# Kernel tuning notes

Hardware: AMD Instinct MI355X
Metric: run time of the kernel (lower is better)

Reference implementation:

```python
import jax, jax.numpy as jnp
import numpy as np
import math

DIM = 1536; NH = 12; HD = 128
F, H, W = 6, 30, 30
S = F * H * W
B = 1
K_LEN = 9900  # hardcoded k_lens in the source forward
EPS_NORM = 1e-6


def _rope_tables(max_len=1024, d=HD):
    # Wan rope_params: three tables of widths d-4*(d//6), 2*(d//6), 2*(d//6)
    # -> cos/sin tables of half-widths 22, 21, 21 (concat = d//2 = 64)
    def ang(dd):
        inv = 1.0 / (10000.0 ** (np.arange(0, dd, 2, dtype=np.float64) / dd))
        return np.outer(np.arange(max_len, dtype=np.float64), inv)
    a = np.concatenate([ang(d - 4 * (d // 6)), ang(2 * (d // 6)), ang(2 * (d // 6))], axis=1)
    return np.cos(a).astype(np.float32), np.sin(a).astype(np.float32)


def setup_inputs() -> dict:
    key = jax.random.key(0)
    ks = jax.random.split(key, 5)
    s = 1.0 / math.sqrt(DIM)
    cos, sin = _rope_tables()
    return {
        "x": jax.random.normal(ks[0], (B, S, DIM), jnp.float32),
        "q_w": jax.random.normal(ks[1], (DIM, DIM), jnp.float32) * s,
        "q_b": jnp.zeros((DIM,), jnp.float32),
        "k_w": jax.random.normal(ks[2], (DIM, DIM), jnp.float32) * s,
        "k_b": jnp.zeros((DIM,), jnp.float32),
        "v_w": jax.random.normal(ks[3], (DIM, DIM), jnp.float32) * s,
        "v_b": jnp.zeros((DIM,), jnp.float32),
        "o_w": jax.random.normal(ks[4], (DIM, DIM), jnp.float32) * s,
        "o_b": jnp.zeros((DIM,), jnp.float32),
        "norm_q_w": jnp.ones((DIM,), jnp.float32),
        "norm_k_w": jnp.ones((DIM,), jnp.float32),
        "freqs_cos": jnp.asarray(cos),
        "freqs_sin": jnp.asarray(sin),
        "grid_f": F, "grid_h": H, "grid_w": W,
    }


def rms_norm(x, w):
    # RMSNorm over full model dim, computed in fp32 (as in source)
    xf = x.astype(jnp.float32)
    xn = xf * jax.lax.rsqrt(jnp.mean(xf * xf, axis=-1, keepdims=True) + EPS_NORM)
    return xn.astype(x.dtype) * w


def rope_apply(x, cos, sin, f, h, w):
    # x: [B,S,N,D]; rotate consecutive pairs with 3D-factorized (f,h,w) freqs
    Bb, Ss, Nn, Dd = x.shape
    c = Dd // 2
    sp = [c - 2 * (c // 3), c // 3, c // 3]  # 22, 21, 21

    def grid(tab):
        tf = tab[:, :sp[0]]
        th = tab[:, sp[0]:sp[0] + sp[1]]
        tw = tab[:, sp[0] + sp[1]:]
        g = jnp.concatenate([
            jnp.broadcast_to(tf[:f, None, None, :], (f, h, w, sp[0])),
            jnp.broadcast_to(th[None, :h, None, :], (f, h, w, sp[1])),
            jnp.broadcast_to(tw[None, None, :w, :], (f, h, w, sp[2])),
        ], axis=-1)
        return g.reshape(f * h * w, 1, c)  # [S,1,c] (broadcast over heads)

    gc, gs = grid(cos), grid(sin)
    xp = x.astype(jnp.float32).reshape(Bb, Ss, Nn, c, 2)
    xr, xi = xp[..., 0], xp[..., 1]
    orr = xr * gc - xi * gs
    oii = xr * gs + xi * gc
    return jnp.stack([orr, oii], axis=-1).reshape(Bb, Ss, Nn, Dd).astype(x.dtype)


def attention(q, k, v, k_len):
    # full attention (window_size=(-1,-1)) with keys masked beyond k_len
    scale = 1.0 / math.sqrt(q.shape[-1])
    att = jnp.einsum('bqnd,bknd->bnqk', q, k) * scale
    valid = jnp.arange(k.shape[1]) < k_len
    att = jnp.where(valid[None, None, None, :], att, jnp.finfo(att.dtype).min)
    p = jax.nn.softmax(att, axis=-1)
    return jnp.einsum('bnqk,bknd->bqnd', p, v)


def reference(x, q_w, q_b, k_w, k_b, v_w, v_b, o_w, o_b, norm_q_w, norm_k_w, freqs_cos, freqs_sin, grid_f, grid_h, grid_w):
    Bb, Ss, _ = x.shape
    q = rms_norm(x @ q_w.T + q_b, norm_q_w).reshape(Bb, Ss, NH, HD)
    k = rms_norm(x @ k_w.T + k_b, norm_k_w).reshape(Bb, Ss, NH, HD)
    v = (x @ v_w.T + v_b).reshape(Bb, Ss, NH, HD)
    q = rope_apply(q, freqs_cos, freqs_sin, grid_f, grid_h, grid_w)
    k = rope_apply(k, freqs_cos, freqs_sin, grid_f, grid_h, grid_w)
    o = attention(q, k, v, K_LEN).reshape(Bb, Ss, NH * HD)
    return o @ o_w.T + o_b
```

## Files before the change

kernel.cpp:

```cpp
#include <hip/hip_runtime.h>

#define DIM 1536
#define NH 12
#define HD 128
#define S_LEN 5400
#define SPAD 5440
#define MPAD 5504
#define NQKV 4608
#define EPS_NORM 1e-6f

typedef __bf16 bf16_t;
typedef __bf16 bf16x8 __attribute__((ext_vector_type(8)));
typedef __bf16 bf16x4 __attribute__((ext_vector_type(4)));
typedef float  f32x4  __attribute__((ext_vector_type(4)));
typedef float  f32x16 __attribute__((ext_vector_type(16)));

#define GLOAD_LDS16(gp, lp) __builtin_amdgcn_global_load_lds( \
    (__attribute__((address_space(1))) void*)(void*)(gp),     \
    (__attribute__((address_space(3))) void*)(lp), 16, 0, 0)


__global__ __launch_bounds__(256) void cvt_x_kernel(const float* __restrict__ x,
                                                    bf16_t* __restrict__ xb) {
  size_t base = ((size_t)blockIdx.x * 256 + threadIdx.x) * 4;
  if (base >= (size_t)MPAD * DIM) return;
  size_t row = base / DIM;
  float4 v = make_float4(0.f, 0.f, 0.f, 0.f);
  if (row < S_LEN) v = *(const float4*)&x[base];
  bf16x4 o; o[0] = (__bf16)v.x; o[1] = (__bf16)v.y; o[2] = (__bf16)v.z; o[3] = (__bf16)v.w;
  *(bf16x4*)&xb[base] = o;
}

__global__ __launch_bounds__(256) void cvt_wqkv_kernel(const float* __restrict__ qw,
                                                       const float* __restrict__ kw,
                                                       const float* __restrict__ vw,
                                                       bf16_t* __restrict__ wb) {
  size_t base = ((size_t)blockIdx.x * 256 + threadIdx.x) * 4;
  if (base >= (size_t)NQKV * DIM) return;
  int row = (int)(base / DIM);
  int col = (int)(base - (size_t)row * DIM);
  const float* src; int rr = row;
  if (rr >= 3072)      { src = vw; rr -= 3072; }
  else if (rr >= 1536) { src = kw; rr -= 1536; }
  else                 { src = qw; }
  float4 v = *(const float4*)&src[(size_t)rr * DIM + col];
  bf16x4 o; o[0] = (__bf16)v.x; o[1] = (__bf16)v.y; o[2] = (__bf16)v.z; o[3] = (__bf16)v.w;
  *(bf16x4*)&wb[base] = o;
}

__global__ __launch_bounds__(256) void cvt_wo_kernel(const float* __restrict__ w,
                                                     bf16_t* __restrict__ wb) {
  size_t base = ((size_t)blockIdx.x * 256 + threadIdx.x) * 4;
  if (base >= (size_t)DIM * DIM) return;
  float4 v = *(const float4*)&w[base];
  bf16x4 o; o[0] = (__bf16)v.x; o[1] = (__bf16)v.y; o[2] = (__bf16)v.z; o[3] = (__bf16)v.w;
  *(bf16x4*)&wb[base] = o;
}


template<bool OUT_BF16>
__global__ __launch_bounds__(256) void gemm_bt_kernel(
    const bf16_t* __restrict__ A, const bf16_t* __restrict__ B, void* __restrict__ C,
    const float* __restrict__ bias0, const float* __restrict__ bias1,
    const float* __restrict__ bias2, int M, int N, int K, int Mvalid) {
  __shared__ bf16_t As[128 * 32];
  __shared__ bf16_t Bs[128 * 32];
  int tid = threadIdx.x;
  int lane = tid & 63, wave = tid >> 6, quad = lane >> 4, l16 = lane & 15;
  int m0 = blockIdx.y * 128, n0 = blockIdx.x * 128;
  int wm = (wave >> 1) * 64, wn = (wave & 1) * 64;
  const bf16_t* Ab = A + (size_t)m0 * K;
  const bf16_t* Bb = B + (size_t)n0 * K;
  f32x4 acc[4][4] = {};
  for (int kt = 0; kt < K; kt += 32) {
    __syncthreads();
#pragma unroll
    for (int i = 0; i < 2; i++) {
      int eo = (i * 256 + tid) * 8;
      int row = eo >> 5, col = eo & 31;
      GLOAD_LDS16(Ab + (size_t)row * K + kt + col, &As[eo]);
      GLOAD_LDS16(Bb + (size_t)row * K + kt + col, &Bs[eo]);
    }
    __syncthreads();
    bf16x8 af[4], bfr[4];
#pragma unroll
    for (int i = 0; i < 4; i++)
      af[i] = *(const bf16x8*)&As[(wm + i * 16 + l16) * 32 + quad * 8];
#pragma unroll
    for (int j = 0; j < 4; j++)
      bfr[j] = *(const bf16x8*)&Bs[(wn + j * 16 + l16) * 32 + quad * 8];
#pragma unroll
    for (int i = 0; i < 4; i++)
#pragma unroll
      for (int j = 0; j < 4; j++)
        acc[i][j] = __builtin_amdgcn_mfma_f32_16x16x32_bf16(af[i], bfr[j], acc[i][j], 0, 0, 0);
  }
#pragma unroll
  for (int j = 0; j < 4; j++) {
    int n = n0 + wn + j * 16 + l16;
    float bias = (n < 1536) ? bias0[n] : (n < 3072) ? bias1[n - 1536] : bias2[n - 3072];
#pragma unroll
    for (int i = 0; i < 4; i++) {
#pragma unroll
      for (int r = 0; r < 4; r++) {
        int m = m0 + wm + i * 16 + quad * 4 + r;
        float v = acc[i][j][r] + bias;
        if (OUT_BF16) {
          ((bf16_t*)C)[(size_t)m * N + n] = (__bf16)v;
        } else {
          if (m < Mvalid) ((float*)C)[(size_t)m * N + n] = v;
        }
      }
    }
  }
}


__global__ __launch_bounds__(256) void rope_qk_kernel(
    const bf16_t* __restrict__ qkv, const float* __restrict__ nqw,
    const float* __restrict__ nkw, const float* __restrict__ fcos,
    const float* __restrict__ fsin, bf16_t* __restrict__ qout,
    bf16_t* __restrict__ kout) {
  int s = blockIdx.x;
  int tid = threadIdx.x;
  bool valid = s < S_LEN;
  int f = s / 900, hh = (s / 30) % 30, ww = s % 30;
  __shared__ float red[4];
  for (int which = 0; which < 2; which++) {
    const bf16_t* src = qkv + (size_t)s * NQKV + which * DIM;
    const float* nw = which ? nkw : nqw;
    bf16_t* dst = (which ? kout : qout) + (size_t)s * DIM;
    float osc = which ? 1.0f : 0.08838834764831845f;
    float v[6]; float ss = 0.f;
#pragma unroll
    for (int i = 0; i < 6; i++) {
      v[i] = valid ? (float)src[tid * 6 + i] : 0.f;
      ss += v[i] * v[i];
    }
#pragma unroll
    for (int off = 32; off >= 1; off >>= 1) ss += __shfl_down(ss, off);
    if ((tid & 63) == 0) red[tid >> 6] = ss;
    __syncthreads();
    float tot = red[0] + red[1] + red[2] + red[3];
    float rn = rsqrtf(tot * (1.f / DIM) + EPS_NORM);
    __syncthreads();
#pragma unroll
    for (int i = 0; i < 3; i++) {
      int e0 = tid * 6 + 2 * i;
      int p = e0 >> 1;
      int cc = p & 63;
      int pos = (cc < 22) ? f : (cc < 43) ? hh : ww;
      float c = fcos[pos * 64 + cc], sn = fsin[pos * 64 + cc];
      float xr = v[2 * i] * rn * nw[e0];
      float xi = v[2 * i + 1] * rn * nw[e0 + 1];
      dst[e0]     = (__bf16)((xr * c - xi * sn) * osc);
      dst[e0 + 1] = (__bf16)((xr * sn + xi * c) * osc);
    }
  }
}


__global__ __launch_bounds__(256) void v_transpose_kernel(const bf16_t* __restrict__ qkv,
                                                          bf16_t* __restrict__ vt) {
  __shared__ bf16_t tile[64][136];
  int h = blockIdx.y, s0 = blockIdx.x * 64, tid = threadIdx.x;
#pragma unroll
  for (int it = 0; it < 4; it++) {
    int eo = (it * 256 + tid) * 8;
    int row = eo >> 7, col = eo & 127;
    int s = s0 + row;
    bf16x8 val = {};
    if (s < S_LEN) val = *(const bf16x8*)&qkv[(size_t)s * NQKV + 3072 + h * HD + col];
    *(bf16x8*)&tile[row][col] = val;
  }
  __syncthreads();
  int d = tid & 127, j0 = (tid >> 7) * 32;
  bf16x8 outv[4];
#pragma unroll
  for (int b = 0; b < 4; b++)
#pragma unroll
    for (int j = 0; j < 8; j++) outv[b][j] = tile[j0 + b * 8 + j][d];
  size_t base = ((size_t)h * HD + d) * SPAD + s0 + j0;
#pragma unroll
  for (int b = 0; b < 4; b++) *(bf16x8*)&vt[base + b * 8] = outv[b];
}


__global__ __launch_bounds__(256, 2) void flash_attn_kernel(
    const bf16_t* __restrict__ q, const bf16_t* __restrict__ k,
    const bf16_t* __restrict__ vt, bf16_t* __restrict__ o) {
  __shared__ bf16_t Ks[64 * 128];
  __shared__ bf16_t Vs[64 * 128];
  __shared__ bf16_t Pw[4][32 * 64];
  int head = blockIdx.y;
  int s0 = blockIdx.x * 128;
  int tid = threadIdx.x, w = tid >> 6, lane = tid & 63;
  int l31 = lane & 31, hh = lane >> 5;

  bf16x8 bq[8];
  {
    const bf16_t* qp = &q[(size_t)(s0 + w * 32 + l31) * DIM + head * HD + hh * 8];
#pragma unroll
    for (int kc = 0; kc < 8; kc++) bq[kc] = *(const bf16x8*)(qp + kc * 16);
  }

  float m_i = -1e30f, l_i = 0.f;
  f32x16 oacc[4] = {};

  for (int kt = 0; kt < SPAD; kt += 64) {
    __syncthreads();
#pragma unroll
    for (int it = 0; it < 4; it++) {
      int slot = it * 256 + tid;
      int row = slot >> 4, pc = slot & 15;
      int c = pc ^ (row & 15);
      GLOAD_LDS16(k + (size_t)(kt + row) * DIM + head * HD + c * 8, &Ks[slot * 8]);
    }
#pragma unroll
    for (int it = 0; it < 4; it++) {
      int slot = it * 256 + tid;
      int row = slot >> 4, pc = slot & 15;
      int cp = pc ^ (row & 15);
      int d = 2 * row + (cp >> 3);
      GLOAD_LDS16(vt + ((size_t)head * HD + d) * SPAD + kt + (cp & 7) * 8, &Vs[slot * 8]);
    }
    __syncthreads();

    f32x16 sacc[2] = {};
#pragma unroll
    for (int ns = 0; ns < 2; ns++) {
      int row = ns * 32 + l31;
#pragma unroll
      for (int kc = 0; kc < 8; kc++) {
        int pc = (kc * 2 + hh) ^ (row & 15);
        bf16x8 ak = *(const bf16x8*)&Ks[row * 128 + pc * 8];
        sacc[ns] = __builtin_amdgcn_mfma_f32_32x32x16_bf16(ak, bq[kc], sacc[ns], 0, 0, 0);
      }
    }

    if (kt + 64 > S_LEN) {
#pragma unroll
      for (int ns = 0; ns < 2; ns++)
#pragma unroll
        for (int r = 0; r < 16; r++) {
          int kvg = kt + ns * 32 + (r & 3) + 8 * (r >> 2) + 4 * hh;
          if (kvg >= S_LEN) sacc[ns][r] = -1e30f;
        }
    }

    float mx = -1e30f;
#pragma unroll
    for (int ns = 0; ns < 2; ns++)
#pragma unroll
      for (int r = 0; r < 16; r++) mx = fmaxf(mx, sacc[ns][r]);
    mx = fmaxf(mx, __shfl_xor(mx, 32));
    float mn = fmaxf(m_i, mx);
    float al = __expf(m_i - mn);
    m_i = mn;
    float rs = 0.f;
#pragma unroll
    for (int ns = 0; ns < 2; ns++)
#pragma unroll
      for (int r = 0; r < 16; r++) {
        float p = __expf(sacc[ns][r] - mn);
        rs += p;
        sacc[ns][r] = p;
      }
    rs += __shfl_xor(rs, 32);
    l_i = l_i * al + rs;
#pragma unroll
    for (int dt = 0; dt < 4; dt++)
#pragma unroll
      for (int r = 0; r < 16; r++) oacc[dt][r] *= al;

#pragma unroll
    for (int ns = 0; ns < 2; ns++)
#pragma unroll
      for (int t = 0; t < 4; t++) {
        bf16x4 pk;
#pragma unroll
        for (int r4 = 0; r4 < 4; r4++) pk[r4] = (__bf16)sacc[ns][t * 4 + r4];
        int c8 = ns * 8 + 2 * t + hh;
        int pc8 = c8 ^ (l31 & 15);
        *(bf16x4*)&Pw[w][l31 * 64 + pc8 * 4] = pk;
      }

#pragma unroll
    for (int kvc = 0; kvc < 4; kvc++) {
      int c8a = kvc * 4 + hh * 2;
      bf16x4 plo = *(const bf16x4*)&Pw[w][l31 * 64 + ((c8a) ^ (l31 & 15)) * 4];
      bf16x4 phi = *(const bf16x4*)&Pw[w][l31 * 64 + ((c8a + 1) ^ (l31 & 15)) * 4];
      bf16x8 bp;
#pragma unroll
      for (int j = 0; j < 4; j++) { bp[j] = plo[j]; bp[j + 4] = phi[j]; }
#pragma unroll
      for (int dt = 0; dt < 4; dt++) {
        int d = dt * 32 + l31;
        int r = d >> 1;
        int cp = ((d & 1) << 3) | (kvc * 2 + hh);
        int pc = cp ^ (r & 15);
        bf16x8 av = *(const bf16x8*)&Vs[r * 128 + pc * 8];
        oacc[dt] = __builtin_amdgcn_mfma_f32_32x32x16_bf16(av, bp, oacc[dt], 0, 0, 0);
      }
    }
  }

  float inv = 1.f / l_i;
  int qr = lane >> 1, seg = lane & 1;
  int srow = s0 + w * 32 + qr;
#pragma unroll
  for (int half = 0; half < 2; half++) {
#pragma unroll
    for (int dl = 0; dl < 2; dl++) {
      int dt = half * 2 + dl;
#pragma unroll
      for (int t = 0; t < 4; t++) {
        bf16x4 v;
#pragma unroll
        for (int r4 = 0; r4 < 4; r4++) v[r4] = (__bf16)(oacc[dt][t * 4 + r4] * inv);
        int c8 = dl * 8 + 2 * t + hh;
        int pc8 = c8 ^ (l31 & 15);
        *(bf16x4*)&Pw[w][l31 * 64 + pc8 * 4] = v;
      }
    }
#pragma unroll
    for (int i = 0; i < 4; i++) {
      int c8 = seg * 8 + 2 * i;
      bf16x4 lo = *(const bf16x4*)&Pw[w][qr * 64 + ((c8) ^ (qr & 15)) * 4];
      bf16x4 hi = *(const bf16x4*)&Pw[w][qr * 64 + ((c8 + 1) ^ (qr & 15)) * 4];
      bf16x8 val;
#pragma unroll
      for (int j = 0; j < 4; j++) { val[j] = lo[j]; val[j + 4] = hi[j]; }
      if (srow < S_LEN)
        *(bf16x8*)&o[(size_t)srow * DIM + head * HD + half * 64 + seg * 32 + i * 8] = val;
    }
    __syncthreads();
  }
}


extern "C" void kernel_launch(void* const* d_in, const int* in_sizes, int n_in,
                              void* d_out, int out_size, void* d_ws, size_t ws_size,
                              hipStream_t stream) {
  const float* x    = (const float*)d_in[0];
  const float* q_w  = (const float*)d_in[1];
  const float* q_b  = (const float*)d_in[2];
  const float* k_w  = (const float*)d_in[3];
  const float* k_b  = (const float*)d_in[4];
  const float* v_w  = (const float*)d_in[5];
  const float* v_b  = (const float*)d_in[6];
  const float* o_w  = (const float*)d_in[7];
  const float* o_b  = (const float*)d_in[8];
  const float* nqw  = (const float*)d_in[9];
  const float* nkw  = (const float*)d_in[10];
  const float* fcos = (const float*)d_in[11];
  const float* fsin = (const float*)d_in[12];

  char* ws = (char*)d_ws;
  bf16_t* xb   = (bf16_t*)(ws + 0);
  bf16_t* wqkv = (bf16_t*)(ws + 16908288);
  bf16_t* wob  = (bf16_t*)(ws + 31064064);
  bf16_t* qkv  = (bf16_t*)(ws + 35782656);
  bf16_t* qb   = (bf16_t*)(ws + 86507520);
  bf16_t* kb   = (bf16_t*)(ws + 103415808);
  bf16_t* vtb  = (bf16_t*)(ws + 0);
  bf16_t* aob  = (bf16_t*)(ws + 35782656);

  cvt_x_kernel<<<(MPAD * DIM / 4 + 255) / 256, 256, 0, stream>>>(x, xb);
  cvt_wqkv_kernel<<<(NQKV * DIM / 4 + 255) / 256, 256, 0, stream>>>(q_w, k_w, v_w, wqkv);
  cvt_wo_kernel<<<(DIM * DIM / 4 + 255) / 256, 256, 0, stream>>>(o_w, wob);

  gemm_bt_kernel<true><<<dim3(NQKV / 128, MPAD / 128), 256, 0, stream>>>(
      xb, wqkv, qkv, q_b, k_b, v_b, MPAD, NQKV, DIM, MPAD);

  rope_qk_kernel<<<MPAD, 256, 0, stream>>>(qkv, nqw, nkw, fcos, fsin, qb, kb);
  v_transpose_kernel<<<dim3(SPAD / 64, NH), 256, 0, stream>>>(qkv, vtb);

  flash_attn_kernel<<<dim3(MPAD / 128, NH), 256, 0, stream>>>(qb, kb, vtb, aob);

  gemm_bt_kernel<false><<<dim3(DIM / 128, MPAD / 128), 256, 0, stream>>>(
      aob, wob, d_out, o_b, o_b, o_b, MPAD, DIM, DIM, S_LEN);
}
```

Baseline: 692.0 us.

## Double-buffer K tiles, load V fragments directly to registers, vectorize rope

The flash attention kernel now double-buffers K tiles in LDS, so the next tile's async load overlaps the current tile's compute, and drops one barrier per iteration. V fragments are loaded straight from global memory into registers instead of being staged through LDS, with the loads split around the QK MFMAs to hide latency. The rope/norm kernel switches to 192 threads doing 8-element vectorized loads and stores. The direct V loads raise register pressure and are less coalesced than the LDS path, which could cost occupancy or bandwidth.

```diff
diff --git a/kernel.cpp b/kernel.cpp
--- a/kernel.cpp
+++ b/kernel.cpp
@@ -116,46 +116,48 @@
 }
 
 
-__global__ __launch_bounds__(256) void rope_qk_kernel(
+__global__ __launch_bounds__(192) void rope_qk_kernel(
     const bf16_t* __restrict__ qkv, const float* __restrict__ nqw,
     const float* __restrict__ nkw, const float* __restrict__ fcos,
     const float* __restrict__ fsin, bf16_t* __restrict__ qout,
     bf16_t* __restrict__ kout) {
   int s = blockIdx.x;
-  int tid = threadIdx.x;
+  int t = threadIdx.x;
   bool valid = s < S_LEN;
   int f = s / 900, hh = (s / 30) % 30, ww = s % 30;
-  __shared__ float red[4];
+  __shared__ float red[3];
   for (int which = 0; which < 2; which++) {
     const bf16_t* src = qkv + (size_t)s * NQKV + which * DIM;
     const float* nw = which ? nkw : nqw;
     bf16_t* dst = (which ? kout : qout) + (size_t)s * DIM;
     float osc = which ? 1.0f : 0.08838834764831845f;
-    float v[6]; float ss = 0.f;
-#pragma unroll
-    for (int i = 0; i < 6; i++) {
-      v[i] = valid ? (float)src[tid * 6 + i] : 0.f;
-      ss += v[i] * v[i];
-    }
+    bf16x8 v8 = {};
+    if (valid) v8 = *(const bf16x8*)&src[t * 8];
+    float v[8]; float ss = 0.f;
+#pragma unroll
+    for (int i = 0; i < 8; i++) { v[i] = (float)v8[i]; ss += v[i] * v[i]; }
 #pragma unroll
     for (int off = 32; off >= 1; off >>= 1) ss += __shfl_down(ss, off);
-    if ((tid & 63) == 0) red[tid >> 6] = ss;
-    __syncthreads();
-    float tot = red[0] + red[1] + red[2] + red[3];
+    if ((t & 63) == 0) red[t >> 6] = ss;
+    __syncthreads();
+    float tot = red[0] + red[1] + red[2];
     float rn = rsqrtf(tot * (1.f / DIM) + EPS_NORM);
     __syncthreads();
-#pragma unroll
-    for (int i = 0; i < 3; i++) {
-      int e0 = tid * 6 + 2 * i;
-      int p = e0 >> 1;
-      int cc = p & 63;
+    const float4* nwp = (const float4*)&nw[t * 8];
+    float4 na = nwp[0], nb = nwp[1];
+    float nwv[8] = {na.x, na.y, na.z, na.w, nb.x, nb.y, nb.z, nb.w};
+    bf16x8 o8;
+#pragma unroll
+    for (int j = 0; j < 4; j++) {
+      int cc = (t * 4 + j) & 63;
       int pos = (cc < 22) ? f : (cc < 43) ? hh : ww;
       float c = fcos[pos * 64 + cc], sn = fsin[pos * 64 + cc];
-      float xr = v[2 * i] * rn * nw[e0];
-      float xi = v[2 * i + 1] * rn * nw[e0 + 1];
-      dst[e0]     = (__bf16)((xr * c - xi * sn) * osc);
-      dst[e0 + 1] = (__bf16)((xr * sn + xi * c) * osc);
-    }
+      float xr = v[2 * j] * rn * nwv[2 * j];
+      float xi = v[2 * j + 1] * rn * nwv[2 * j + 1];
+      o8[2 * j]     = (__bf16)((xr * c - xi * sn) * osc);
+      o8[2 * j + 1] = (__bf16)((xr * sn + xi * c) * osc);
+    }
+    *(bf16x8*)&dst[t * 8] = o8;
   }
 }
 
@@ -189,8 +191,7 @@
 __global__ __launch_bounds__(256, 2) void flash_attn_kernel(
     const bf16_t* __restrict__ q, const bf16_t* __restrict__ k,
     const bf16_t* __restrict__ vt, bf16_t* __restrict__ o) {
-  __shared__ bf16_t Ks[64 * 128];
-  __shared__ bf16_t Vs[64 * 128];
+  __shared__ bf16_t Ks2[2][64 * 128];
   __shared__ bf16_t Pw[4][32 * 64];
   int head = blockIdx.y;
   int s0 = blockIdx.x * 128;
@@ -204,27 +205,34 @@
     for (int kc = 0; kc < 8; kc++) bq[kc] = *(const bf16x8*)(qp + kc * 16);
   }
 
-  float m_i = -1e30f, l_i = 0.f;
-  f32x16 oacc[4] = {};
-
-  for (int kt = 0; kt < SPAD; kt += 64) {
-    __syncthreads();
+  auto stage = [&](int buf, int kt) {
 #pragma unroll
     for (int it = 0; it < 4; it++) {
       int slot = it * 256 + tid;
       int row = slot >> 4, pc = slot & 15;
       int c = pc ^ (row & 15);
-      GLOAD_LDS16(k + (size_t)(kt + row) * DIM + head * HD + c * 8, &Ks[slot * 8]);
-    }
-#pragma unroll
-    for (int it = 0; it < 4; it++) {
-      int slot = it * 256 + tid;
-      int row = slot >> 4, pc = slot & 15;
-      int cp = pc ^ (row & 15);
-      int d = 2 * row + (cp >> 3);
-      GLOAD_LDS16(vt + ((size_t)head * HD + d) * SPAD + kt + (cp & 7) * 8, &Vs[slot * 8]);
-    }
-    __syncthreads();
+      GLOAD_LDS16(k + (size_t)(kt + row) * DIM + head * HD + c * 8, &Ks2[buf][slot * 8]);
+    }
+  };
+  stage(0, 0);
+
+  const bf16_t* vbase = vt + (size_t)head * HD * SPAD;
+  float m_i = -1e30f, l_i = 0.f;
+  f32x16 oacc[4] = {};
+
+  for (int it85 = 0; it85 < 85; it85++) {
+    int kt = it85 * 64;
+    int buf = it85 & 1;
+    __syncthreads();
+    if (it85 + 1 < 85) stage(buf ^ 1, kt + 64);
+    const bf16_t* Ks = Ks2[buf];
+
+    bf16x8 av[16];
+#pragma unroll
+    for (int i = 0; i < 8; i++) {
+      int kvc = i >> 2, dt = i & 3;
+      av[i] = *(const bf16x8*)&vbase[(size_t)(dt * 32 + l31) * SPAD + kt + kvc * 16 + hh * 8];
+    }
 
     f32x16 sacc[2] = {};
 #pragma unroll
@@ -236,6 +244,12 @@
         bf16x8 ak = *(const bf16x8*)&Ks[row * 128 + pc * 8];
         sacc[ns] = __builtin_amdgcn_mfma_f32_32x32x16_bf16(ak, bq[kc], sacc[ns], 0, 0, 0);
       }
+    }
+
+#pragma unroll
+    for (int i = 8; i < 16; i++) {
+      int kvc = i >> 2, dt = i & 3;
+      av[i] = *(const bf16x8*)&vbase[(size_t)(dt * 32 + l31) * SPAD + kt + kvc * 16 + hh * 8];
     }
 
     if (kt + 64 > S_LEN) {
@@ -294,14 +308,8 @@
 #pragma unroll
       for (int j = 0; j < 4; j++) { bp[j] = plo[j]; bp[j + 4] = phi[j]; }
 #pragma unroll
-      for (int dt = 0; dt < 4; dt++) {
-        int d = dt * 32 + l31;
-        int r = d >> 1;
-        int cp = ((d & 1) << 3) | (kvc * 2 + hh);
-        int pc = cp ^ (r & 15);
-        bf16x8 av = *(const bf16x8*)&Vs[r * 128 + pc * 8];
-        oacc[dt] = __builtin_amdgcn_mfma_f32_32x32x16_bf16(av, bp, oacc[dt], 0, 0, 0);
-      }
+      for (int dt = 0; dt < 4; dt++)
+        oacc[dt] = __builtin_amdgcn_mfma_f32_32x32x16_bf16(av[kvc * 4 + dt], bp, oacc[dt], 0, 0, 0);
     }
   }
 
@@ -334,7 +342,6 @@
       if (srow < S_LEN)
         *(bf16x8*)&o[(size_t)srow * DIM + head * HD + half * 64 + seg * 32 + i * 8] = val;
     }
-    __syncthreads();
   }
 }
 
@@ -373,7 +380,7 @@
   gemm_bt_kernel<true><<<dim3(NQKV / 128, MPAD / 128), 256, 0, stream>>>(
       xb, wqkv, qkv, q_b, k_b, v_b, MPAD, NQKV, DIM, MPAD);
 
-  rope_qk_kernel<<<MPAD, 256, 0, stream>>>(qkv, nqw, nkw, fcos, fsin, qb, kb);
+  rope_qk_kernel<<<MPAD, 192, 0, stream>>>(qkv, nqw, nkw, fcos, fsin, qb, kb);
   v_transpose_kernel<<<dim3(SPAD / 64, NH), 256, 0, stream>>>(qkv, vtb);
 
   flash_attn_kernel<<<dim3(MPAD / 128, NH), 256, 0, stream>>>(qb, kb, vtb, aob);
```

Result: slower. 927.1 us (+34.0%).
